# Optimization experiments

Hardware: AMD Instinct MI355X
Metric: run time of the kernel (lower is better)

Reference implementation:

```python
import jax, jax.numpy as jnp
import numpy as np

N = 131072   # num_nodes
E = 262144   # events in the batch
D = 128      # memory_dim
R = 128      # raw_msg_dim
T = 32       # time_dim


def setup_inputs() -> dict:
    key = jax.random.key(0)
    ks = jax.random.split(key, 16)
    s = 0.05
    return {
        "memory": jax.random.normal(ks[0], (N, D), jnp.float32) * s,
        "raw_msg": jax.random.normal(ks[1], (E, R), jnp.float32) * s,
        "time_w": jax.random.normal(ks[2], (T,), jnp.float32) * s,
        "time_b": jax.random.normal(ks[3], (T,), jnp.float32) * s,
        "W_msg_s": jax.random.normal(ks[4], (D, 2 * D + R + T), jnp.float32) * s,
        "b_msg_s": jax.random.normal(ks[5], (D,), jnp.float32) * s,
        "W_msg_d": jax.random.normal(ks[6], (D, 2 * D + R + T), jnp.float32) * s,
        "b_msg_d": jax.random.normal(ks[7], (D,), jnp.float32) * s,
        "W_ih": jax.random.normal(ks[8], (3 * D, D), jnp.float32) * s,
        "W_hh": jax.random.normal(ks[9], (3 * D, D), jnp.float32) * s,
        "b_ih": jax.random.normal(ks[10], (3 * D,), jnp.float32) * s,
        "b_hh": jax.random.normal(ks[11], (3 * D,), jnp.float32) * s,
        "src": jax.random.randint(ks[12], (E,), 0, N, jnp.int32),
        "dst": jax.random.randint(ks[13], (E,), 0, N, jnp.int32),
        "t": jax.random.randint(ks[14], (E,), 0, 100000, jnp.int32),
        "last_update": jax.random.randint(ks[15], (N,), 0, 50000, jnp.int32),
    }


def _time_enc(t_rel, time_w, time_b):
    # TimeEncoder: cos(Linear(t)) ; t_rel: [E] float -> [E, T]
    return jnp.cos(t_rel[:, None] * time_w[None, :] + time_b[None, :])


def _message(mem_a, mem_b, raw_msg, t_enc, W, b):
    # message MLP on concat(mem_src, mem_dst, raw_msg, t_enc)
    x = jnp.concatenate([mem_a, mem_b, raw_msg, t_enc], axis=-1)  # [E, 2D+R+T]
    return jax.nn.relu(x @ W.T + b)


def _forward(memory, raw_msg, time_w, time_b, W_msg_s, b_msg_s, W_msg_d, b_msg_d,
             W_ih, W_hh, b_ih, b_hh, src, dst, t, last_update):
    tf = t.astype(jnp.float32)
    lu = last_update.astype(jnp.float32)
    mem_s = memory[src]  # gather [E, D]
    mem_d = memory[dst]

    # source-side messages (stored under key src): t_rel = t - last_update[src]
    t_enc_s = _time_enc(tf - lu[src], time_w, time_b)
    msg_s = _message(mem_s, mem_d, raw_msg, t_enc_s, W_msg_s, b_msg_s)
    # dest-side messages (stored under key dst, src/dst swapped)
    t_enc_d = _time_enc(tf - lu[dst], time_w, time_b)
    msg_d = _message(mem_d, mem_s, raw_msg, t_enc_d, W_msg_d, b_msg_d)

    # scatter mean-aggregate messages onto their owner node
    seg = jnp.concatenate([src, dst], axis=0)          # [2E]
    vals = jnp.concatenate([msg_s, msg_d], axis=0)     # [2E, D]
    sums = jax.ops.segment_sum(vals, seg, num_segments=N)
    cnt = jax.ops.segment_sum(jnp.ones((2 * E,), jnp.float32), seg, num_segments=N)
    aggr = sums / jnp.maximum(cnt, 1.0)[:, None]       # [N, D]

    # GRUCell(aggr, memory)
    gi = aggr @ W_ih.T + b_ih
    gh = memory @ W_hh.T + b_hh
    i_r, i_z, i_n = jnp.split(gi, 3, axis=-1)
    h_r, h_z, h_n = jnp.split(gh, 3, axis=-1)
    r = jax.nn.sigmoid(i_r + h_r)
    z = jax.nn.sigmoid(i_z + h_z)
    n = jnp.tanh(i_n + r * h_n)
    new_memory = (1.0 - z) * n + z * memory

    # scatter-max timestamps (pyg scatter reduce='max' fills empty slots with 0)
    tt = jnp.concatenate([t, t], axis=0)
    seg_max = jax.ops.segment_max(tt, seg, num_segments=N)
    new_last_update = jnp.where(cnt > 0, seg_max, jnp.zeros((), jnp.int32))
    return new_memory, new_last_update


def reference(memory, raw_msg, time_w, time_b, W_msg_s, b_msg_s, W_msg_d, b_msg_d,
              W_ih, W_hh, b_ih, b_hh, src, dst, t, last_update):
    return _forward(memory, raw_msg, time_w, time_b, W_msg_s, b_msg_s, W_msg_d,
                    b_msg_d, W_ih, W_hh, b_ih, b_hh, src, dst, t, last_update)
```

## Files before the change

kernel.cpp:

```cpp
#include <hip/hip_runtime.h>
#include <cstdint>
#include <cstddef>

#define NN 131072
#define EE 262144

typedef __attribute__((ext_vector_type(8))) short bf16x8;
typedef __attribute__((ext_vector_type(4))) float f32x4;

__device__ __forceinline__ unsigned short f2bf(float f) {
    unsigned int u = __builtin_bit_cast(unsigned int, f);
    u += 0x7FFFu + ((u >> 16) & 1u);
    return (unsigned short)(u >> 16);
}
__device__ __forceinline__ float bf2f(unsigned short s) {
    unsigned int u = ((unsigned int)s) << 16;
    return __builtin_bit_cast(float, u);
}
__device__ __forceinline__ float sigmoidf_(float x) { return 1.0f / (1.0f + __expf(-x)); }
__device__ __forceinline__ float tanhf_(float x) {
    float ax = fabsf(x);
    float e = __expf(-2.0f * ax);
    return copysignf((1.0f - e) / (1.0f + e), x);
}
__device__ __forceinline__ bf16x8 pack8(const float* f) {
    bf16x8 o;
#pragma unroll
    for (int i = 0; i < 8; ++i) o[i] = (short)f2bf(f[i]);
    return o;
}

__device__ __forceinline__ float wmsg_val(int n, int k, const float* Ws, const float* Wd) {
    if (n < 128) {
        return (k < 416) ? Ws[n * 416 + k] : 0.0f;
    } else {
        int m = n - 128;
        if (k < 128)       return Wd[m * 416 + 128 + k];
        else if (k < 256)  return Wd[m * 416 + (k - 128)];
        else if (k < 384)  return Wd[m * 416 + k];
        else if (k < 416)  return 0.0f;
        else               return Wd[m * 416 + 384 + (k - 416)];
    }
}
__device__ __forceinline__ float wgru_val(int j, int k, const float* Wih, const float* Whh) {
    if (j < 256)      return (k < 128) ? Wih[j * 128 + k] : Whh[j * 128 + (k - 128)];
    else if (j < 384) return (k < 128) ? Wih[j * 128 + k] : 0.0f;
    else              return (k < 128) ? 0.0f : Whh[(j - 128) * 128 + (k - 128)];
}

__global__ void k_prep_msgfrag(const float* __restrict__ Ws, const float* __restrict__ Wd,
                               const float* __restrict__ bs, const float* __restrict__ bd,
                               unsigned short* __restrict__ Wmf, float* __restrict__ bm) {
    int b = blockIdx.x;
    int c = b >> 4, nt = b & 15;
    int lane = threadIdx.x;
    int col0 = lane & 15, q = lane >> 4;
    int n = nt * 16 + col0;
    float f[8];
#pragma unroll
    for (int j = 0; j < 8; ++j) f[j] = wmsg_val(n, c * 32 + q * 8 + j, Ws, Wd);
    ((bf16x8*)Wmf)[(size_t)b * 64 + lane] = pack8(f);
    if (b == 0)
        for (int i = lane; i < 256; i += 64) bm[i] = (i < 128) ? bs[i] : bd[i - 128];
}

__global__ void k_prep_grufrag(const float* __restrict__ Wih, const float* __restrict__ Whh,
                               const float* __restrict__ bih, const float* __restrict__ bhh,
                               unsigned short* __restrict__ Wgf, float* __restrict__ bg) {
    int b = blockIdx.x;
    int c = b >> 5, nt = b & 31;
    int lane = threadIdx.x;
    int col0 = lane & 15, q = lane >> 4;
    int j0 = nt * 16 + col0;
    float f[8];
#pragma unroll
    for (int j = 0; j < 8; ++j) f[j] = wgru_val(j0, c * 32 + q * 8 + j, Wih, Whh);
    ((bf16x8*)Wgf)[(size_t)b * 64 + lane] = pack8(f);
    if (b == 0)
        for (int i = lane; i < 512; i += 64)
            bg[i] = (i < 256) ? (bih[i] + bhh[i]) : ((i < 384) ? bih[i] : bhh[i - 128]);
}

__global__ void k_memconv(const float* __restrict__ in, unsigned short* __restrict__ outp) {
    int gid = blockIdx.x * 256 + threadIdx.x;
    const float4 v = ((const float4*)in)[gid];
    ushort4 o;
    o.x = f2bf(v.x); o.y = f2bf(v.y); o.z = f2bf(v.z); o.w = f2bf(v.w);
    *(ushort4*)(outp + (size_t)gid * 4) = o;
}

__global__ void k_pre(const int* __restrict__ t, const int* __restrict__ src,
                      const int* __restrict__ dst, const int* __restrict__ lu,
                      float* __restrict__ trel_s, float* __restrict__ trel_d,
                      int* cnt, int* lu_tmp) {
    int e = blockIdx.x * 256 + threadIdx.x;
    int s = src[e], d = dst[e], tv = t[e];
    trel_s[e] = (float)(tv - lu[s]);
    trel_d[e] = (float)(tv - lu[d]);
    atomicAdd(&cnt[s], 1);
    atomicAdd(&cnt[d], 1);
    atomicMax(&lu_tmp[s], tv);
    atomicMax(&lu_tmp[d], tv);
}

__global__ void k_scan1(const int* __restrict__ cnt, int* __restrict__ bsum) {
    __shared__ int red[256];
    int tid = threadIdx.x;
    red[tid] = cnt[blockIdx.x * 256 + tid];
    __syncthreads();
    for (int s = 128; s > 0; s >>= 1) {
        if (tid < s) red[tid] += red[tid + s];
        __syncthreads();
    }
    if (tid == 0) bsum[blockIdx.x] = red[0];
}
__global__ void k_scan2(const int* __restrict__ bsum, int* __restrict__ boff) {
    __shared__ int sb[512];
    int tid = threadIdx.x;
    int v = bsum[tid];
    sb[tid] = v;
    __syncthreads();
    for (int d = 1; d < 512; d <<= 1) {
        int u = (tid >= d) ? sb[tid - d] : 0;
        __syncthreads();
        sb[tid] += u;
        __syncthreads();
    }
    boff[tid] = sb[tid] - v;
}
__global__ void k_scan3(const int* __restrict__ cnt, const int* __restrict__ boff,
                        int* __restrict__ off, int* __restrict__ cursor) {
    __shared__ int sb[256];
    int tid = threadIdx.x;
    int i = blockIdx.x * 256 + tid;
    int v = cnt[i];
    sb[tid] = v;
    __syncthreads();
    for (int d = 1; d < 256; d <<= 1) {
        int u = (tid >= d) ? sb[tid - d] : 0;
        __syncthreads();
        sb[tid] += u;
        __syncthreads();
    }
    int o = boff[blockIdx.x] + sb[tid] - v;
    off[i] = o;
    cursor[i] = o;
}
__global__ void k_fill(const int* __restrict__ src, const int* __restrict__ dst,
                       int* cursor, int* __restrict__ pos2) {
    int e2 = blockIdx.x * 256 + threadIdx.x;
    int node = (e2 < EE) ? src[e2] : dst[e2 - EE];
    pos2[e2] = atomicAdd(&cursor[node], 1);
}

__launch_bounds__(256, 3)
__global__ void k_msg(const unsigned short* __restrict__ memb,
                      const float* __restrict__ raw,
                      const float* __restrict__ trel_s,
                      const float* __restrict__ trel_d,
                      const unsigned short* __restrict__ Wmf,
                      const float* __restrict__ bm,
                      const int* __restrict__ src, const int* __restrict__ dst,
                      const int* __restrict__ pos2,
                      const float* __restrict__ tw, const float* __restrict__ tb,
                      unsigned short* __restrict__ msg) {
    __shared__ int s_idx[64], d_idx[64], s_pos[64], d_pos[64];
    __shared__ float s_tw[32], s_tb[32];
    __shared__ __align__(16) unsigned short As[2][64 * 72];

    const int tid = threadIdx.x;
    const int e0 = blockIdx.x * 64;
    if (tid < 64)        { s_idx[tid] = src[e0 + tid];            s_pos[tid] = pos2[e0 + tid]; }
    else if (tid < 128)  { d_idx[tid - 64] = dst[e0 + tid - 64];  d_pos[tid - 64] = pos2[EE + e0 + tid - 64]; }
    else if (tid < 160)  s_tw[tid - 128] = tw[tid - 128];
    else if (tid < 192)  s_tb[tid - 160] = tb[tid - 160];
    __syncthreads();

    const int lane = tid & 63, w = tid >> 6;
    const int col0 = lane & 15, q = lane >> 4;

    const int mrow0 = tid >> 3, mseg = tid & 7;
    const int rrow  = tid >> 4, rseg = tid & 15;
    const int trow  = tid >> 2, tq   = tid & 3;

    float4 p0, p1, p2, p3;

    auto stage_load = [&](int t) {
        if (t < 4) {
            int colb = (t & 1) * 64;
            int n0i = (t < 2) ? s_idx[mrow0] : d_idx[mrow0];
            int n1i = (t < 2) ? s_idx[mrow0 + 32] : d_idx[mrow0 + 32];
            p0 = *(const float4*)(memb + (size_t)n0i * 128 + colb + mseg * 8);
            p1 = *(const float4*)(memb + (size_t)n1i * 128 + colb + mseg * 8);
        } else if (t < 6) {
            const float* rbase = raw + (size_t)e0 * 128 + (t & 1) * 64 + rseg * 4;
            p0 = *(const float4*)(rbase + (size_t)(rrow +  0) * 128);
            p1 = *(const float4*)(rbase + (size_t)(rrow + 16) * 128);
            p2 = *(const float4*)(rbase + (size_t)(rrow + 32) * 128);
            p3 = *(const float4*)(rbase + (size_t)(rrow + 48) * 128);
        } else {
            p0.x = (tq < 2) ? trel_s[e0 + trow] : trel_d[e0 + trow];
        }
    };

    auto stage_write = [&](int t, unsigned short* A) {
        if (t < 4) {
            *(bf16x8*)&A[mrow0 * 72 + mseg * 8]        = __builtin_bit_cast(bf16x8, p0);
            *(bf16x8*)&A[(mrow0 + 32) * 72 + mseg * 8] = __builtin_bit_cast(bf16x8, p1);
        } else if (t < 6) {
            ushort4 o;
            o.x = f2bf(p0.x); o.y = f2bf(p0.y); o.z = f2bf(p0.z); o.w = f2bf(p0.w);
            *(ushort4*)&A[(rrow +  0) * 72 + rseg * 4] = o;
            o.x = f2bf(p1.x); o.y = f2bf(p1.y); o.z = f2bf(p1.z); o.w = f2bf(p1.w);
            *(ushort4*)&A[(rrow + 16) * 72 + rseg * 4] = o;
            o.x = f2bf(p2.x); o.y = f2bf(p2.y); o.z = f2bf(p2.z); o.w = f2bf(p2.w);
            *(ushort4*)&A[(rrow + 32) * 72 + rseg * 4] = o;
            o.x = f2bf(p3.x); o.y = f2bf(p3.y); o.z = f2bf(p3.z); o.w = f2bf(p3.w);
            *(ushort4*)&A[(rrow + 48) * 72 + rseg * 4] = o;
        } else {
            float f[16];
            float tr = p0.x;
#pragma unroll
            for (int j = 0; j < 16; ++j) {
                int jj = (tq & 1) * 16 + j;
                f[j] = __cosf(tr * s_tw[jj] + s_tb[jj]);
            }
            *(bf16x8*)&A[trow * 72 + tq * 16]     = pack8(&f[0]);
            *(bf16x8*)&A[trow * 72 + tq * 16 + 8] = pack8(&f[8]);
        }
    };

    f32x4 acc[4][4];
#pragma unroll
    for (int a = 0; a < 4; ++a)
#pragma unroll
        for (int b = 0; b < 4; ++b)
#pragma unroll
            for (int i = 0; i < 4; ++i) acc[a][b][i] = 0.0f;

    stage_load(0);
    stage_write(0, As[0]);
    stage_load(1);
    __syncthreads();

#pragma unroll
    for (int t = 0; t < 7; ++t) {
        unsigned short* A = As[t & 1];
        if (t < 6) stage_write(t + 1, As[(t + 1) & 1]);
        if (t < 5) stage_load(t + 2);
#pragma unroll
        for (int kk = 0; kk < 2; ++kk) {
            bf16x8 bfr[4];
            const bf16x8* Wc = (const bf16x8*)Wmf + (size_t)(2 * t + kk) * 16 * 64;
#pragma unroll
            for (int nl = 0; nl < 4; ++nl)
                bfr[nl] = Wc[(w * 4 + nl) * 64 + lane];
            bf16x8 afr[4];
#pragma unroll
            for (int mt = 0; mt < 4; ++mt)
                afr[mt] = *(const bf16x8*)&A[(mt * 16 + col0) * 72 + kk * 32 + q * 8];
#pragma unroll
            for (int mt = 0; mt < 4; ++mt)
#pragma unroll
                for (int nl = 0; nl < 4; ++nl)
                    acc[mt][nl] = __builtin_amdgcn_mfma_f32_16x16x32_bf16(afr[mt], bfr[nl], acc[mt][nl], 0, 0, 0);
        }
        __syncthreads();
    }

    unsigned short* scr = &As[0][0] + w * 1280;
    const bool is_s = (w < 2);
#pragma unroll
    for (int mt = 0; mt < 4; ++mt) {
#pragma unroll
        for (int nl = 0; nl < 4; ++nl) {
            int j = (w * 4 + nl) * 16 + col0;
            float bv = bm[j];
            int gl = nl * 2 + (col0 >> 3);
            int ci = col0 & 7;
#pragma unroll
            for (int r = 0; r < 4; ++r) {
                int rr = q * 4 + r;
                float v = fmaxf(acc[mt][nl][r] + bv, 0.0f);
                scr[rr * 80 + ((gl + rr) & 7) * 8 + ci] = f2bf(v);
            }
        }
        asm volatile("s_waitcnt lgkmcnt(0)" ::: "memory");
        {
            int rr2 = lane & 15, p = lane >> 4;
            int ev = mt * 16 + rr2;
            int pos = is_s ? s_pos[ev] : d_pos[ev];
            bf16x8 v0 = *(const bf16x8*)&scr[rr2 * 80 + (((2 * p)     + rr2) & 7) * 8];
            bf16x8 v1 = *(const bf16x8*)&scr[rr2 * 80 + (((2 * p + 1) + rr2) & 7) * 8];
            unsigned short* dstp = msg + (size_t)pos * 128 + (w & 1) * 64 + p * 16;
            *(bf16x8*)dstp = v0;
            *(bf16x8*)(dstp + 8) = v1;
        }
        asm volatile("s_waitcnt lgkmcnt(0)" ::: "memory");
    }
}

__launch_bounds__(256, 2)
__global__ void k_gru(const unsigned short* __restrict__ msg,
                      const int* __restrict__ off, const int* __restrict__ cnt,
                      const float* __restrict__ memory,
                      const unsigned short* __restrict__ Wgf,
                      const float* __restrict__ bg,
                      float* __restrict__ out) {
    __shared__ __align__(16) unsigned short Xs[64 * 264];

    const int tid = threadIdx.x;
    const int n0 = blockIdx.x * 64;

#pragma unroll
    for (int h = 0; h < 2; ++h) {
        int g = tid >> 3, sub = tid & 7;
        int gr = h * 32 + g;
        int node = n0 + gr;
        int beg = off[node], cn = cnt[node];
        float a[16];
#pragma unroll
        for (int i = 0; i < 16; ++i) a[i] = 0.0f;
        for (int m = 0; m < cn; ++m) {
            const bf16x8* p = (const bf16x8*)(msg + (size_t)(beg + m) * 128 + sub * 16);
            bf16x8 v0 = p[0], v1 = p[1];
#pragma unroll
            for (int k = 0; k < 8; ++k) {
                a[k]     += bf2f((unsigned short)v0[k]);
                a[8 + k] += bf2f((unsigned short)v1[k]);
            }
        }
        float inv = 1.0f / (float)(cn > 1 ? cn : 1);
#pragma unroll
        for (int i = 0; i < 16; ++i) a[i] *= inv;
        *(bf16x8*)&Xs[gr * 264 + sub * 16] = pack8(&a[0]);
        *(bf16x8*)&Xs[gr * 264 + sub * 16 + 8] = pack8(&a[8]);
        float f[16];
        const float4* mp = (const float4*)(memory + (size_t)node * 128 + sub * 16);
#pragma unroll
        for (int s = 0; s < 4; ++s) {
            float4 v = mp[s];
            f[s * 4 + 0] = v.x; f[s * 4 + 1] = v.y; f[s * 4 + 2] = v.z; f[s * 4 + 3] = v.w;
        }
        *(bf16x8*)&Xs[gr * 264 + 128 + sub * 16] = pack8(&f[0]);
        *(bf16x8*)&Xs[gr * 264 + 128 + sub * 16 + 8] = pack8(&f[8]);
    }
    __syncthreads();

    const int lane = tid & 63, w = tid >> 6;
    const int col0 = lane & 15, q = lane >> 4;

    f32x4 acc[4][4][2];
#pragma unroll
    for (int a = 0; a < 4; ++a)
#pragma unroll
        for (int g = 0; g < 4; ++g)
#pragma unroll
            for (int f = 0; f < 2; ++f)
#pragma unroll
                for (int i = 0; i < 4; ++i) acc[a][g][f][i] = 0.0f;

#pragma unroll
    for (int c = 0; c < 8; ++c) {
        bf16x8 bfr[4][2];
        const bf16x8* Wc = (const bf16x8*)Wgf + (size_t)c * 32 * 64;
#pragma unroll
        for (int g = 0; g < 4; ++g)
#pragma unroll
            for (int fh = 0; fh < 2; ++fh)
                bfr[g][fh] = Wc[(8 * g + 2 * w + fh) * 64 + lane];
        bf16x8 afr[4];
#pragma unroll
        for (int mt = 0; mt < 4; ++mt)
            afr[mt] = *(const bf16x8*)&Xs[(mt * 16 + col0) * 264 + c * 32 + q * 8];
#pragma unroll
        for (int mt = 0; mt < 4; ++mt)
#pragma unroll
            for (int g = 0; g < 4; ++g)
#pragma unroll
                for (int fh = 0; fh < 2; ++fh)
                    acc[mt][g][fh] = __builtin_amdgcn_mfma_f32_16x16x32_bf16(afr[mt], bfr[g][fh], acc[mt][g][fh], 0, 0, 0);
    }

#pragma unroll
    for (int fh = 0; fh < 2; ++fh) {
        int feat = w * 32 + fh * 16 + col0;
        float b_r = bg[feat], b_z = bg[128 + feat], b_in = bg[256 + feat], b_hn = bg[384 + feat];
#pragma unroll
        for (int mt = 0; mt < 4; ++mt) {
#pragma unroll
            for (int r = 0; r < 4; ++r) {
                int node = n0 + mt * 16 + q * 4 + r;
                float rr = sigmoidf_(acc[mt][0][fh][r] + b_r);
                float zz = sigmoidf_(acc[mt][1][fh][r] + b_z);
                float nn = tanhf_((acc[mt][2][fh][r] + b_in) + rr * (acc[mt][3][fh][r] + b_hn));
                float h = memory[(size_t)node * 128 + feat];
                out[(size_t)node * 128 + feat] = (1.0f - zz) * nn + zz * h;
            }
        }
    }
}

__global__ void k_lu(const int* __restrict__ lu_tmp, float* __restrict__ outp) {
    int i = blockIdx.x * 256 + threadIdx.x;
    outp[i] = (float)lu_tmp[i];
}

extern "C" void kernel_launch(void* const* d_in, const int* in_sizes, int n_in,
                              void* d_out, int out_size, void* d_ws, size_t ws_size,
                              hipStream_t stream) {
    const float* memory = (const float*)d_in[0];
    const float* raw    = (const float*)d_in[1];
    const float* tw     = (const float*)d_in[2];
    const float* tb     = (const float*)d_in[3];
    const float* Wms    = (const float*)d_in[4];
    const float* bms    = (const float*)d_in[5];
    const float* Wmd    = (const float*)d_in[6];
    const float* bmd    = (const float*)d_in[7];
    const float* Wih    = (const float*)d_in[8];
    const float* Whh    = (const float*)d_in[9];
    const float* bih    = (const float*)d_in[10];
    const float* bhh    = (const float*)d_in[11];
    const int* src = (const int*)d_in[12];
    const int* dst = (const int*)d_in[13];
    const int* t   = (const int*)d_in[14];
    const int* lu  = (const int*)d_in[15];

    char* ws = (char*)d_ws;
    size_t ob = 0;
    unsigned short* memb = (unsigned short*)(ws + ob); ob += (size_t)NN * 128 * 2;
    unsigned short* msg  = (unsigned short*)(ws + ob); ob += (size_t)2 * EE * 128 * 2;
    float* trel_s        = (float*)(ws + ob);          ob += (size_t)EE * 4;
    float* trel_d        = (float*)(ws + ob);          ob += (size_t)EE * 4;
    int* cnt             = (int*)(ws + ob);            ob += (size_t)NN * 4;
    int* off             = (int*)(ws + ob);            ob += (size_t)NN * 4;
    int* cursor          = (int*)(ws + ob);            ob += (size_t)NN * 4;
    int* lu_tmp          = (int*)(ws + ob);            ob += (size_t)NN * 4;
    int* pos2            = (int*)(ws + ob);            ob += (size_t)2 * EE * 4;
    int* bsum            = (int*)(ws + ob);            ob += 512 * 4;
    int* boff            = (int*)(ws + ob);            ob += 512 * 4;
    unsigned short* Wmf  = (unsigned short*)(ws + ob); ob += (size_t)14 * 16 * 64 * 8 * 2;
    float* bm            = (float*)(ws + ob);          ob += 256 * 4;
    unsigned short* Wgf  = (unsigned short*)(ws + ob); ob += (size_t)8 * 32 * 64 * 8 * 2;
    float* bg            = (float*)(ws + ob);          ob += 512 * 4;

    float* out = (float*)d_out;

    hipMemsetAsync(cnt, 0, (size_t)NN * 4, stream);
    hipMemsetAsync(lu_tmp, 0, (size_t)NN * 4, stream);

    k_prep_msgfrag<<<14 * 16, 64, 0, stream>>>(Wms, Wmd, bms, bmd, Wmf, bm);
    k_prep_grufrag<<<8 * 32, 64, 0, stream>>>(Wih, Whh, bih, bhh, Wgf, bg);
    k_memconv<<<(NN * 128 / 4) / 256, 256, 0, stream>>>(memory, memb);
    k_pre<<<EE / 256, 256, 0, stream>>>(t, src, dst, lu, trel_s, trel_d, cnt, lu_tmp);
    k_scan1<<<512, 256, 0, stream>>>(cnt, bsum);
    k_scan2<<<1, 512, 0, stream>>>(bsum, boff);
    k_scan3<<<512, 256, 0, stream>>>(cnt, boff, off, cursor);
    k_fill<<<2 * EE / 256, 256, 0, stream>>>(src, dst, cursor, pos2);
    k_msg<<<EE / 64, 256, 0, stream>>>(memb, raw, trel_s, trel_d, Wmf, bm, src, dst, pos2, tw, tb, msg);
    k_gru<<<NN / 64, 256, 0, stream>>>(msg, off, cnt, memory, Wgf, bg, out);
    k_lu<<<NN / 256, 256, 0, stream>>>(lu_tmp, out + (size_t)NN * 128);
}
```

Baseline: 552.2 us.

## Load MFMA A-fragments directly from global memory, dropping LDS staging

The message kernel used to gather memory rows, raw messages and time encodings into a double-buffered LDS tile before the MFMA loop. It now has each wave load its A fragments straight from global memory into registers, converting and computing cos in registers, and it removes the per-stage barriers. This cuts LDS traffic and synchronisation and shrinks shared memory, which may raise occupancy. In exchange, all four waves load the same A data redundantly from global memory/L2, the access pattern is less coalesced, and the explicit prefetch pipelining is gone.

```diff
diff --git a/kernel.cpp b/kernel.cpp
--- a/kernel.cpp
+++ b/kernel.cpp
@@ -164,111 +164,93 @@
                       const int* __restrict__ pos2,
                       const float* __restrict__ tw, const float* __restrict__ tb,
                       unsigned short* __restrict__ msg) {
-    __shared__ int s_idx[64], d_idx[64], s_pos[64], d_pos[64];
-    __shared__ float s_tw[32], s_tb[32];
-    __shared__ __align__(16) unsigned short As[2][64 * 72];
+    __shared__ int s_pos[64], d_pos[64];
+    __shared__ __align__(16) unsigned short scr_all[4 * 1280];
 
     const int tid = threadIdx.x;
     const int e0 = blockIdx.x * 64;
-    if (tid < 64)        { s_idx[tid] = src[e0 + tid];            s_pos[tid] = pos2[e0 + tid]; }
-    else if (tid < 128)  { d_idx[tid - 64] = dst[e0 + tid - 64];  d_pos[tid - 64] = pos2[EE + e0 + tid - 64]; }
-    else if (tid < 160)  s_tw[tid - 128] = tw[tid - 128];
-    else if (tid < 192)  s_tb[tid - 160] = tb[tid - 160];
-    __syncthreads();
+    if (tid < 64)        s_pos[tid] = pos2[e0 + tid];
+    else if (tid < 128)  d_pos[tid - 64] = pos2[EE + e0 + tid - 64];
 
     const int lane = tid & 63, w = tid >> 6;
     const int col0 = lane & 15, q = lane >> 4;
 
-    const int mrow0 = tid >> 3, mseg = tid & 7;
-    const int rrow  = tid >> 4, rseg = tid & 15;
-    const int trow  = tid >> 2, tq   = tid & 3;
-
-    float4 p0, p1, p2, p3;
-
-    auto stage_load = [&](int t) {
-        if (t < 4) {
-            int colb = (t & 1) * 64;
-            int n0i = (t < 2) ? s_idx[mrow0] : d_idx[mrow0];
-            int n1i = (t < 2) ? s_idx[mrow0 + 32] : d_idx[mrow0 + 32];
-            p0 = *(const float4*)(memb + (size_t)n0i * 128 + colb + mseg * 8);
-            p1 = *(const float4*)(memb + (size_t)n1i * 128 + colb + mseg * 8);
-        } else if (t < 6) {
-            const float* rbase = raw + (size_t)e0 * 128 + (t & 1) * 64 + rseg * 4;
-            p0 = *(const float4*)(rbase + (size_t)(rrow +  0) * 128);
-            p1 = *(const float4*)(rbase + (size_t)(rrow + 16) * 128);
-            p2 = *(const float4*)(rbase + (size_t)(rrow + 32) * 128);
-            p3 = *(const float4*)(rbase + (size_t)(rrow + 48) * 128);
+    int sn[4], dn[4];
+#pragma unroll
+    for (int mt = 0; mt < 4; ++mt) {
+        int ev = mt * 16 + col0;
+        sn[mt] = src[e0 + ev];
+        dn[mt] = dst[e0 + ev];
+    }
+    const float4 tw0 = *(const float4*)(tw + q * 8);
+    const float4 tw1 = *(const float4*)(tw + q * 8 + 4);
+    const float4 tb0 = *(const float4*)(tb + q * 8);
+    const float4 tb1 = *(const float4*)(tb + q * 8 + 4);
+
+    __syncthreads();
+
+    f32x4 acc[4][4];
+#pragma unroll
+    for (int a = 0; a < 4; ++a)
+#pragma unroll
+        for (int b = 0; b < 4; ++b)
+#pragma unroll
+            for (int i = 0; i < 4; ++i) acc[a][b][i] = 0.0f;
+
+#pragma unroll
+    for (int c = 0; c < 14; ++c) {
+        bf16x8 bfr[4];
+        const bf16x8* Wc = (const bf16x8*)Wmf + (size_t)c * 16 * 64;
+#pragma unroll
+        for (int nl = 0; nl < 4; ++nl)
+            bfr[nl] = Wc[(w * 4 + nl) * 64 + lane];
+
+        bf16x8 afr[4];
+        if (c < 8) {
+            const int cb = (c & 3) * 32 + q * 8;
+#pragma unroll
+            for (int mt = 0; mt < 4; ++mt) {
+                int node = (c < 4) ? sn[mt] : dn[mt];
+                afr[mt] = *(const bf16x8*)(memb + (size_t)node * 128 + cb);
+            }
+        } else if (c < 12) {
+            const int cb = (c - 8) * 32 + q * 8;
+#pragma unroll
+            for (int mt = 0; mt < 4; ++mt) {
+                int ev = mt * 16 + col0;
+                const float* rp = raw + (size_t)(e0 + ev) * 128 + cb;
+                const float4 a = *(const float4*)rp;
+                const float4 b = *(const float4*)(rp + 4);
+                float f[8] = {a.x, a.y, a.z, a.w, b.x, b.y, b.z, b.w};
+                afr[mt] = pack8(f);
+            }
         } else {
-            p0.x = (tq < 2) ? trel_s[e0 + trow] : trel_d[e0 + trow];
-        }
-    };
-
-    auto stage_write = [&](int t, unsigned short* A) {
-        if (t < 4) {
-            *(bf16x8*)&A[mrow0 * 72 + mseg * 8]        = __builtin_bit_cast(bf16x8, p0);
-            *(bf16x8*)&A[(mrow0 + 32) * 72 + mseg * 8] = __builtin_bit_cast(bf16x8, p1);
-        } else if (t < 6) {
-            ushort4 o;
-            o.x = f2bf(p0.x); o.y = f2bf(p0.y); o.z = f2bf(p0.z); o.w = f2bf(p0.w);
-            *(ushort4*)&A[(rrow +  0) * 72 + rseg * 4] = o;
-            o.x = f2bf(p1.x); o.y = f2bf(p1.y); o.z = f2bf(p1.z); o.w = f2bf(p1.w);
-            *(ushort4*)&A[(rrow + 16) * 72 + rseg * 4] = o;
-            o.x = f2bf(p2.x); o.y = f2bf(p2.y); o.z = f2bf(p2.z); o.w = f2bf(p2.w);
-            *(ushort4*)&A[(rrow + 32) * 72 + rseg * 4] = o;
-            o.x = f2bf(p3.x); o.y = f2bf(p3.y); o.z = f2bf(p3.z); o.w = f2bf(p3.w);
-            *(ushort4*)&A[(rrow + 48) * 72 + rseg * 4] = o;
-        } else {
-            float f[16];
-            float tr = p0.x;
-#pragma unroll
-            for (int j = 0; j < 16; ++j) {
-                int jj = (tq & 1) * 16 + j;
-                f[j] = __cosf(tr * s_tw[jj] + s_tb[jj]);
-            }
-            *(bf16x8*)&A[trow * 72 + tq * 16]     = pack8(&f[0]);
-            *(bf16x8*)&A[trow * 72 + tq * 16 + 8] = pack8(&f[8]);
-        }
-    };
-
-    f32x4 acc[4][4];
-#pragma unroll
-    for (int a = 0; a < 4; ++a)
-#pragma unroll
-        for (int b = 0; b < 4; ++b)
-#pragma unroll
-            for (int i = 0; i < 4; ++i) acc[a][b][i] = 0.0f;
-
-    stage_load(0);
-    stage_write(0, As[0]);
-    stage_load(1);
-    __syncthreads();
-
-#pragma unroll
-    for (int t = 0; t < 7; ++t) {
-        unsigned short* A = As[t & 1];
-        if (t < 6) stage_write(t + 1, As[(t + 1) & 1]);
-        if (t < 5) stage_load(t + 2);
-#pragma unroll
-        for (int kk = 0; kk < 2; ++kk) {
-            bf16x8 bfr[4];
-            const bf16x8* Wc = (const bf16x8*)Wmf + (size_t)(2 * t + kk) * 16 * 64;
+            const float* trp = (c == 12) ? trel_s : trel_d;
+#pragma unroll
+            for (int mt = 0; mt < 4; ++mt) {
+                int ev = mt * 16 + col0;
+                float tr = trp[e0 + ev];
+                float f[8];
+                f[0] = __cosf(tr * tw0.x + tb0.x);
+                f[1] = __cosf(tr * tw0.y + tb0.y);
+                f[2] = __cosf(tr * tw0.z + tb0.z);
+                f[3] = __cosf(tr * tw0.w + tb0.w);
+                f[4] = __cosf(tr * tw1.x + tb1.x);
+                f[5] = __cosf(tr * tw1.y + tb1.y);
+                f[6] = __cosf(tr * tw1.z + tb1.z);
+                f[7] = __cosf(tr * tw1.w + tb1.w);
+                afr[mt] = pack8(f);
+            }
+        }
+
+#pragma unroll
+        for (int mt = 0; mt < 4; ++mt)
 #pragma unroll
             for (int nl = 0; nl < 4; ++nl)
-                bfr[nl] = Wc[(w * 4 + nl) * 64 + lane];
-            bf16x8 afr[4];
-#pragma unroll
-            for (int mt = 0; mt < 4; ++mt)
-                afr[mt] = *(const bf16x8*)&A[(mt * 16 + col0) * 72 + kk * 32 + q * 8];
-#pragma unroll
-            for (int mt = 0; mt < 4; ++mt)
-#pragma unroll
-                for (int nl = 0; nl < 4; ++nl)
-                    acc[mt][nl] = __builtin_amdgcn_mfma_f32_16x16x32_bf16(afr[mt], bfr[nl], acc[mt][nl], 0, 0, 0);
-        }
-        __syncthreads();
-    }
-
-    unsigned short* scr = &As[0][0] + w * 1280;
+                acc[mt][nl] = __builtin_amdgcn_mfma_f32_16x16x32_bf16(afr[mt], bfr[nl], acc[mt][nl], 0, 0, 0);
+    }
+
+    unsigned short* scr = scr_all + w * 1280;
     const bool is_s = (w < 2);
 #pragma unroll
     for (int mt = 0; mt < 4; ++mt) {
```

Result: slower. 648.8 us (+17.5%).

## Widen message-GEMM K stages to 128 and use lighter LDS barriers

Applied to the files above, without the earlier changes.

The message kernel's shared A tile grows from 64-wide to 128-wide K slices, so the concatenated input is staged in 4 pipeline steps instead of 7. Each thread issues more loads per stage, and the loop runs more MFMA chunks per stage, which means fewer block-wide barriers. __syncthreads is replaced by an explicit lgkmcnt wait plus s_barrier. The cost is roughly double the LDS footprint and more live registers (eight float4 prefetch values), which may reduce occupancy under launch_bounds(256,3).

```diff
diff --git a/kernel.cpp b/kernel.cpp
--- a/kernel.cpp
+++ b/kernel.cpp
@@ -166,7 +166,7 @@
                       unsigned short* __restrict__ msg) {
     __shared__ int s_idx[64], d_idx[64], s_pos[64], d_pos[64];
     __shared__ float s_tw[32], s_tb[32];
-    __shared__ __align__(16) unsigned short As[2][64 * 72];
+    __shared__ __align__(16) unsigned short As[2][64 * 136];
 
     const int tid = threadIdx.x;
     const int e0 = blockIdx.x * 64;
@@ -179,44 +179,58 @@
     const int lane = tid & 63, w = tid >> 6;
     const int col0 = lane & 15, q = lane >> 4;
 
-    const int mrow0 = tid >> 3, mseg = tid & 7;
-    const int rrow  = tid >> 4, rseg = tid & 15;
-    const int trow  = tid >> 2, tq   = tid & 3;
-
-    float4 p0, p1, p2, p3;
+    const int mrow = tid >> 4, mseg = tid & 15;
+    const int rrow = tid >> 5, rseg = tid & 31;
+    const int trow = tid >> 2, tq   = tid & 3;
+
+    float4 p0, p1, p2, p3, p4, p5, p6, p7;
 
     auto stage_load = [&](int t) {
-        if (t < 4) {
-            int colb = (t & 1) * 64;
-            int n0i = (t < 2) ? s_idx[mrow0] : d_idx[mrow0];
-            int n1i = (t < 2) ? s_idx[mrow0 + 32] : d_idx[mrow0 + 32];
-            p0 = *(const float4*)(memb + (size_t)n0i * 128 + colb + mseg * 8);
-            p1 = *(const float4*)(memb + (size_t)n1i * 128 + colb + mseg * 8);
-        } else if (t < 6) {
-            const float* rbase = raw + (size_t)e0 * 128 + (t & 1) * 64 + rseg * 4;
+        if (t < 2) {
+            const int* idx = (t == 0) ? s_idx : d_idx;
+            p0 = *(const float4*)(memb + (size_t)idx[mrow +  0] * 128 + mseg * 8);
+            p1 = *(const float4*)(memb + (size_t)idx[mrow + 16] * 128 + mseg * 8);
+            p2 = *(const float4*)(memb + (size_t)idx[mrow + 32] * 128 + mseg * 8);
+            p3 = *(const float4*)(memb + (size_t)idx[mrow + 48] * 128 + mseg * 8);
+        } else if (t == 2) {
+            const float* rbase = raw + (size_t)e0 * 128 + rseg * 4;
             p0 = *(const float4*)(rbase + (size_t)(rrow +  0) * 128);
-            p1 = *(const float4*)(rbase + (size_t)(rrow + 16) * 128);
-            p2 = *(const float4*)(rbase + (size_t)(rrow + 32) * 128);
-            p3 = *(const float4*)(rbase + (size_t)(rrow + 48) * 128);
+            p1 = *(const float4*)(rbase + (size_t)(rrow +  8) * 128);
+            p2 = *(const float4*)(rbase + (size_t)(rrow + 16) * 128);
+            p3 = *(const float4*)(rbase + (size_t)(rrow + 24) * 128);
+            p4 = *(const float4*)(rbase + (size_t)(rrow + 32) * 128);
+            p5 = *(const float4*)(rbase + (size_t)(rrow + 40) * 128);
+            p6 = *(const float4*)(rbase + (size_t)(rrow + 48) * 128);
+            p7 = *(const float4*)(rbase + (size_t)(rrow + 56) * 128);
         } else {
             p0.x = (tq < 2) ? trel_s[e0 + trow] : trel_d[e0 + trow];
         }
     };
 
     auto stage_write = [&](int t, unsigned short* A) {
-        if (t < 4) {
-            *(bf16x8*)&A[mrow0 * 72 + mseg * 8]        = __builtin_bit_cast(bf16x8, p0);
-            *(bf16x8*)&A[(mrow0 + 32) * 72 + mseg * 8] = __builtin_bit_cast(bf16x8, p1);
-        } else if (t < 6) {
+        if (t < 2) {
+            *(bf16x8*)&A[(mrow +  0) * 136 + mseg * 8] = __builtin_bit_cast(bf16x8, p0);
+            *(bf16x8*)&A[(mrow + 16) * 136 + mseg * 8] = __builtin_bit_cast(bf16x8, p1);
+            *(bf16x8*)&A[(mrow + 32) * 136 + mseg * 8] = __builtin_bit_cast(bf16x8, p2);
+            *(bf16x8*)&A[(mrow + 48) * 136 + mseg * 8] = __builtin_bit_cast(bf16x8, p3);
+        } else if (t == 2) {
             ushort4 o;
             o.x = f2bf(p0.x); o.y = f2bf(p0.y); o.z = f2bf(p0.z); o.w = f2bf(p0.w);
-            *(ushort4*)&A[(rrow +  0) * 72 + rseg * 4] = o;
+            *(ushort4*)&A[(rrow +  0) * 136 + rseg * 4] = o;
             o.x = f2bf(p1.x); o.y = f2bf(p1.y); o.z = f2bf(p1.z); o.w = f2bf(p1.w);
-            *(ushort4*)&A[(rrow + 16) * 72 + rseg * 4] = o;
+            *(ushort4*)&A[(rrow +  8) * 136 + rseg * 4] = o;
             o.x = f2bf(p2.x); o.y = f2bf(p2.y); o.z = f2bf(p2.z); o.w = f2bf(p2.w);
-            *(ushort4*)&A[(rrow + 32) * 72 + rseg * 4] = o;
+            *(ushort4*)&A[(rrow + 16) * 136 + rseg * 4] = o;
             o.x = f2bf(p3.x); o.y = f2bf(p3.y); o.z = f2bf(p3.z); o.w = f2bf(p3.w);
-            *(ushort4*)&A[(rrow + 48) * 72 + rseg * 4] = o;
+            *(ushort4*)&A[(rrow + 24) * 136 + rseg * 4] = o;
+            o.x = f2bf(p4.x); o.y = f2bf(p4.y); o.z = f2bf(p4.z); o.w = f2bf(p4.w);
+            *(ushort4*)&A[(rrow + 32) * 136 + rseg * 4] = o;
+            o.x = f2bf(p5.x); o.y = f2bf(p5.y); o.z = f2bf(p5.z); o.w = f2bf(p5.w);
+            *(ushort4*)&A[(rrow + 40) * 136 + rseg * 4] = o;
+            o.x = f2bf(p6.x); o.y = f2bf(p6.y); o.z = f2bf(p6.z); o.w = f2bf(p6.w);
+            *(ushort4*)&A[(rrow + 48) * 136 + rseg * 4] = o;
+            o.x = f2bf(p7.x); o.y = f2bf(p7.y); o.z = f2bf(p7.z); o.w = f2bf(p7.w);
+            *(ushort4*)&A[(rrow + 56) * 136 + rseg * 4] = o;
         } else {
             float f[16];
             float tr = p0.x;
@@ -225,8 +239,8 @@
                 int jj = (tq & 1) * 16 + j;
                 f[j] = __cosf(tr * s_tw[jj] + s_tb[jj]);
             }
-            *(bf16x8*)&A[trow * 72 + tq * 16]     = pack8(&f[0]);
-            *(bf16x8*)&A[trow * 72 + tq * 16 + 8] = pack8(&f[8]);
+            *(bf16x8*)&A[trow * 136 + tq * 16]     = pack8(&f[0]);
+            *(bf16x8*)&A[trow * 136 + tq * 16 + 8] = pack8(&f[8]);
         }
     };
 
@@ -241,31 +255,36 @@
     stage_load(0);
     stage_write(0, As[0]);
     stage_load(1);
-    __syncthreads();
-
-#pragma unroll
-    for (int t = 0; t < 7; ++t) {
-        unsigned short* A = As[t & 1];
-        if (t < 6) stage_write(t + 1, As[(t + 1) & 1]);
-        if (t < 5) stage_load(t + 2);
-#pragma unroll
-        for (int kk = 0; kk < 2; ++kk) {
+    asm volatile("s_waitcnt lgkmcnt(0)" ::: "memory");
+    __builtin_amdgcn_s_barrier();
+
+#pragma unroll
+    for (int t = 0; t < 4; ++t) {
+        const unsigned short* A = As[t & 1];
+        if (t < 3) stage_write(t + 1, As[(t + 1) & 1]);
+        if (t < 2) stage_load(t + 2);
+        const int nkk = (t == 3) ? 2 : 4;
+#pragma unroll
+        for (int kk = 0; kk < 4; ++kk) {
+            if (kk >= nkk) break;
+            const int c = (t < 3) ? (t * 4 + kk) : (12 + kk);
             bf16x8 bfr[4];
-            const bf16x8* Wc = (const bf16x8*)Wmf + (size_t)(2 * t + kk) * 16 * 64;
+            const bf16x8* Wc = (const bf16x8*)Wmf + (size_t)c * 16 * 64;
 #pragma unroll
             for (int nl = 0; nl < 4; ++nl)
                 bfr[nl] = Wc[(w * 4 + nl) * 64 + lane];
             bf16x8 afr[4];
 #pragma unroll
             for (int mt = 0; mt < 4; ++mt)
-                afr[mt] = *(const bf16x8*)&A[(mt * 16 + col0) * 72 + kk * 32 + q * 8];
+                afr[mt] = *(const bf16x8*)&A[(mt * 16 + col0) * 136 + kk * 32 + q * 8];
 #pragma unroll
             for (int mt = 0; mt < 4; ++mt)
 #pragma unroll
                 for (int nl = 0; nl < 4; ++nl)
                     acc[mt][nl] = __builtin_amdgcn_mfma_f32_16x16x32_bf16(afr[mt], bfr[nl], acc[mt][nl], 0, 0, 0);
         }
-        __syncthreads();
+        asm volatile("s_waitcnt lgkmcnt(0)" ::: "memory");
+        __builtin_amdgcn_s_barrier();
     }
 
     unsigned short* scr = &As[0][0] + w * 1280;
```

New measurement: 547.6 us. Within noise of the previous version (-0.8%).
